# Kernel optimization log

Hardware: AMD Instinct MI355X
Metric: run time of the kernel (lower is better)

The kernel has to match this reference:

```python
import jax, jax.numpy as jnp
import numpy as np

B, IN_DIM, D, C = 16384, 1024, 256, 100


def setup_inputs() -> dict:
    key = jax.random.key(0)
    k1, k2, k3, k4 = jax.random.split(key, 4)
    x = jax.random.normal(k1, (B, IN_DIM), dtype=jnp.float32)
    W = jax.random.normal(k2, (IN_DIM, D), dtype=jnp.float32) * (1.0 / np.sqrt(IN_DIM))
    b = jax.random.normal(k3, (D,), dtype=jnp.float32) * 0.01
    P = jax.random.normal(k4, (C, D), dtype=jnp.float32)  # class prototypes [C, D]
    return {"x": x, "W": W, "b": b, "P": P}


def reference(x, W, b, P):
    # Encoder: Z = x @ W + b  -> [B, D]
    Z = x @ W + b
    d = Z.shape[-1]
    # MSE(r, p) = mean((r - p)^2) = (|r|^2 - 2 r.p + |p|^2) / D
    # Computed via expansion to avoid the [B, C, D] broadcast intermediate.
    sq = (
        jnp.sum(Z * Z, axis=-1, keepdims=True)      # [B, 1]
        - 2.0 * (Z @ P.T)                            # [B, C]
        + jnp.sum(P * P, axis=-1)[None, :]           # [1, C]
    )
    return -sq / d  # [B, C]
```

## Files before the change

### kernel.cpp

```cpp
#include <hip/hip_runtime.h>

#define BATCH 16384
#define KDIM  1024
#define DDIM  256
#define CNUM  100
#define CPAD  112
#define RSTR  72

typedef __bf16 bf16x8 __attribute__((ext_vector_type(8)));
typedef float  floatx4 __attribute__((ext_vector_type(4)));

static __device__ __forceinline__ unsigned short f2b(float f) {
    return __builtin_bit_cast(unsigned short, (__bf16)f);
}

__global__ __launch_bounds__(256) void prep(const float* __restrict__ W,
                                            const float* __restrict__ P,
                                            unsigned short* __restrict__ Wt2,
                                            unsigned short* __restrict__ Pbf,
                                            float* __restrict__ pnorm2) {
    __shared__ float T[32][33];
    const int bid = blockIdx.x;
    if (bid < 256) {
        const int k0 = (bid & 31) * 32;
        const int n0 = (bid >> 5) * 32;
        const int j  = threadIdx.x & 31;
        const int i0 = threadIdx.x >> 5;
#pragma unroll
        for (int l = 0; l < 4; ++l) {
            int i = i0 + l * 8;
            T[i][j] = W[(k0 + i) * DDIM + n0 + j];
        }
        __syncthreads();
        if (threadIdx.x < 128) {
            const int l  = threadIdx.x & 63;
            const int fn = threadIdx.x >> 6;
            const int lm = l & 15, lq = l >> 4;
            bf16x8 v;
#pragma unroll
            for (int jj = 0; jj < 8; ++jj)
                v[jj] = (__bf16)T[lq * 8 + jj][fn * 16 + lm];
            const int nblk = (n0 >> 4) + fn;
            const int kblk = k0 >> 5;
            *(bf16x8*)&Wt2[(nblk * 32 + kblk) * 512 + l * 8] = v;
        }
    } else {
        const int wave = threadIdx.x >> 6;
        const int lane = threadIdx.x & 63;
        const int c = (bid - 256) * 4 + wave;
        float s = 0.f;
#pragma unroll
        for (int jj = 0; jj < 4; ++jj) {
            int d = jj * 64 + lane;
            float v = (c < CNUM) ? P[c * DDIM + d] : 0.f;
            Pbf[c * DDIM + d] = f2b(v);
            s += v * v;
        }
#pragma unroll
        for (int m = 1; m < 64; m <<= 1) s += __shfl_xor(s, m, 64);
        if (lane == 0) pnorm2[c] = s;
    }
}

#define KSTEP(KK, CUR, NXT, P0, P1, P2, P3)                                    \
    {                                                                          \
        const unsigned short* As_c = U16 + (CUR) * 8192 + kh * 4096;           \
        const int kb_ = (KK) >> 5;                                             \
        if ((KK) + 64 < 512) {                                                 \
            _Pragma("unroll")                                                  \
            for (int kf = 0; kf < 2; ++kf) {                                   \
                _Pragma("unroll")                                              \
                for (int f = 0; f < 4; ++f)                                    \
                    b[NXT][kf * 4 + f] = *(const bf16x8*)(gB + f * 16384 +     \
                                                     (kb_ + 2 + kf) * 512);    \
            }                                                                  \
            bf16x8 ha;                                                         \
            ha[0] = (__bf16)P0[0]; ha[1] = (__bf16)P0[1];                      \
            ha[2] = (__bf16)P0[2]; ha[3] = (__bf16)P0[3];                      \
            ha[4] = (__bf16)P1[0]; ha[5] = (__bf16)P1[1];                      \
            ha[6] = (__bf16)P1[2]; ha[7] = (__bf16)P1[3];                      \
            *(bf16x8*)&U16[(NXT) * 8192 + ldsA] = ha;                          \
            bf16x8 hb;                                                         \
            hb[0] = (__bf16)P2[0]; hb[1] = (__bf16)P2[1];                      \
            hb[2] = (__bf16)P2[2]; hb[3] = (__bf16)P2[3];                      \
            hb[4] = (__bf16)P3[0]; hb[5] = (__bf16)P3[1];                      \
            hb[6] = (__bf16)P3[2]; hb[7] = (__bf16)P3[3];                      \
            *(bf16x8*)&U16[(NXT) * 8192 + 4096 + ldsA] = hb;                   \
            if ((KK) + 192 < 512) {                                            \
                P0 = *(const floatx4*)(gA + (KK) + 192);                       \
                P1 = *(const floatx4*)(gA + (KK) + 196);                       \
                P2 = *(const floatx4*)(gA + 512 + (KK) + 192);                 \
                P3 = *(const floatx4*)(gA + 512 + (KK) + 196);                 \
            }                                                                  \
        }                                                                      \
        _Pragma("unroll")                                                      \
        for (int kf = 0; kf < 2; ++kf) {                                       \
            const int sw = kf ? sw1 : sw0;                                     \
            bf16x8 a0 = *(const bf16x8*)&As_c[lm * 64 + sw];                   \
            bf16x8 a1 = *(const bf16x8*)&As_c[(16 + lm) * 64 + sw];            \
            bf16x8 a2 = *(const bf16x8*)&As_c[(32 + lm) * 64 + sw];            \
            bf16x8 a3 = *(const bf16x8*)&As_c[(48 + lm) * 64 + sw];            \
            _Pragma("unroll")                                                  \
            for (int f = 0; f < 4; ++f) {                                      \
                acc[0][f] = __builtin_amdgcn_mfma_f32_16x16x32_bf16(           \
                    a0, b[CUR][kf * 4 + f], acc[0][f], 0, 0, 0);               \
                acc[1][f] = __builtin_amdgcn_mfma_f32_16x16x32_bf16(           \
                    a1, b[CUR][kf * 4 + f], acc[1][f], 0, 0, 0);               \
                acc[2][f] = __builtin_amdgcn_mfma_f32_16x16x32_bf16(           \
                    a2, b[CUR][kf * 4 + f], acc[2][f], 0, 0, 0);               \
                acc[3][f] = __builtin_amdgcn_mfma_f32_16x16x32_bf16(           \
                    a3, b[CUR][kf * 4 + f], acc[3][f], 0, 0, 0);               \
            }                                                                  \
        }                                                                      \
        asm volatile("s_waitcnt lgkmcnt(0)\n\ts_barrier" ::: "memory");        \
    }

__global__ __launch_bounds__(512, 2) void fused_main(
    const float* __restrict__ x, const float* __restrict__ bias,
    const unsigned short* __restrict__ Wt2, const unsigned short* __restrict__ Pbf,
    const float* __restrict__ pnorm2, float* __restrict__ out)
{
    __shared__ __align__(16) float Ubuf[4 * 64 * RSTR];
    __shared__ float rn2[4][64];
    unsigned short* U16 = (unsigned short*)Ubuf;
    float* Rs = Ubuf;
    unsigned short* Zs = (unsigned short*)Ubuf;

    const int tid  = threadIdx.x;
    const int wave = tid >> 6;
    const int kh   = wave >> 2;
    const int wn   = wave & 3;
    const int lane = tid & 63;
    const int lm   = lane & 15;
    const int lq   = lane >> 4;
    const int r0   = blockIdx.x * 64;

    const int rowA = tid >> 3;
    const int kbA  = tid & 7;
    const float* gA = x + (size_t)(r0 + rowA) * KDIM + kbA * 8;
    const int ldsA = rowA * 64 + ((kbA ^ (rowA & 7)) * 8);

    const unsigned short* gB = Wt2 + wn * 65536 + kh * 8192 + lane * 8;

    const int sw0 = ((0 * 4 + lq) ^ (lm & 7)) * 8;
    const int sw1 = ((1 * 4 + lq) ^ (lm & 7)) * 8;

    floatx4 acc[4][4];
#pragma unroll
    for (int g = 0; g < 4; ++g)
#pragma unroll
        for (int f = 0; f < 4; ++f) { acc[g][f][0]=0.f; acc[g][f][1]=0.f; acc[g][f][2]=0.f; acc[g][f][3]=0.f; }

    bf16x8 b[2][8];

    {
        floatx4 q0 = *(const floatx4*)(gA);
        floatx4 q1 = *(const floatx4*)(gA + 4);
        floatx4 q2 = *(const floatx4*)(gA + 512);
        floatx4 q3 = *(const floatx4*)(gA + 516);
        bf16x8 ha;
        ha[0] = (__bf16)q0[0]; ha[1] = (__bf16)q0[1];
        ha[2] = (__bf16)q0[2]; ha[3] = (__bf16)q0[3];
        ha[4] = (__bf16)q1[0]; ha[5] = (__bf16)q1[1];
        ha[6] = (__bf16)q1[2]; ha[7] = (__bf16)q1[3];
        *(bf16x8*)&U16[ldsA] = ha;
        bf16x8 hb;
        hb[0] = (__bf16)q2[0]; hb[1] = (__bf16)q2[1];
        hb[2] = (__bf16)q2[2]; hb[3] = (__bf16)q2[3];
        hb[4] = (__bf16)q3[0]; hb[5] = (__bf16)q3[1];
        hb[6] = (__bf16)q3[2]; hb[7] = (__bf16)q3[3];
        *(bf16x8*)&U16[4096 + ldsA] = hb;
    }
#pragma unroll
    for (int kf = 0; kf < 2; ++kf)
#pragma unroll
        for (int f = 0; f < 4; ++f)
            b[0][kf * 4 + f] = *(const bf16x8*)(gB + f * 16384 + kf * 512);
    floatx4 pa0 = *(const floatx4*)(gA + 64);
    floatx4 pa1 = *(const floatx4*)(gA + 68);
    floatx4 pa2 = *(const floatx4*)(gA + 576);
    floatx4 pa3 = *(const floatx4*)(gA + 580);
    floatx4 pb0 = *(const floatx4*)(gA + 128);
    floatx4 pb1 = *(const floatx4*)(gA + 132);
    floatx4 pb2 = *(const floatx4*)(gA + 640);
    floatx4 pb3 = *(const floatx4*)(gA + 644);
    asm volatile("s_waitcnt lgkmcnt(0)\n\ts_barrier" ::: "memory");

    for (int kk0 = 0; kk0 < 512; kk0 += 128) {
        KSTEP(kk0,      0, 1, pa0, pa1, pa2, pa3)
        KSTEP(kk0 + 64, 1, 0, pb0, pb1, pb2, pb3)
    }

    if (kh == 1) {
#pragma unroll
        for (int g = 0; g < 4; ++g)
#pragma unroll
            for (int f = 0; f < 4; ++f)
                *(floatx4*)&Rs[(wn * 64 + f * 16 + lm) * RSTR + g * 16 + lq * 4] = acc[g][f];
    }
    __syncthreads();
    if (kh == 0) {
#pragma unroll
        for (int g = 0; g < 4; ++g)
#pragma unroll
            for (int f = 0; f < 4; ++f) {
                floatx4 p = *(const floatx4*)&Rs[(wn * 64 + f * 16 + lm) * RSTR + g * 16 + lq * 4];
#pragma unroll
                for (int r = 0; r < 4; ++r) acc[g][f][r] += p[r];
            }
#pragma unroll
        for (int f = 0; f < 4; ++f) {
            float bb = bias[wn * 64 + f * 16 + lm];
#pragma unroll
            for (int g = 0; g < 4; ++g)
#pragma unroll
                for (int r = 0; r < 4; ++r) acc[g][f][r] += bb;
        }
#pragma unroll
        for (int g = 0; g < 4; ++g) {
            float s0 = 0.f, s1 = 0.f, s2 = 0.f, s3 = 0.f;
#pragma unroll
            for (int f = 0; f < 4; ++f) {
                s0 += acc[g][f][0] * acc[g][f][0];
                s1 += acc[g][f][1] * acc[g][f][1];
                s2 += acc[g][f][2] * acc[g][f][2];
                s3 += acc[g][f][3] * acc[g][f][3];
            }
#pragma unroll
            for (int m = 1; m < 16; m <<= 1) {
                s0 += __shfl_xor(s0, m, 64);
                s1 += __shfl_xor(s1, m, 64);
                s2 += __shfl_xor(s2, m, 64);
                s3 += __shfl_xor(s3, m, 64);
            }
            if (lm == 0) {
                int rl = g * 16 + lq * 4;
                rn2[wn][rl + 0] = s0;
                rn2[wn][rl + 1] = s1;
                rn2[wn][rl + 2] = s2;
                rn2[wn][rl + 3] = s3;
            }
        }
    }
    __syncthreads();

    if (kh == 0) {
#pragma unroll
        for (int g = 0; g < 4; ++g)
#pragma unroll
            for (int f = 0; f < 4; ++f) {
                int col = wn * 64 + f * 16 + lm;
#pragma unroll
                for (int r = 0; r < 4; ++r)
                    Zs[(g * 16 + lq * 4 + r) * 264 + col] = f2b(acc[g][f][r]);
            }
    }
    __syncthreads();

    {
        const int ct = wave;
        if (ct < 7) {
            floatx4 acc2[4];
#pragma unroll
            for (int nf = 0; nf < 4; ++nf) { acc2[nf][0]=0.f; acc2[nf][1]=0.f; acc2[nf][2]=0.f; acc2[nf][3]=0.f; }
            const unsigned short* gP = Pbf + (ct * 16 + lm) * DDIM + lq * 8;
#pragma unroll
            for (int ks = 0; ks < 8; ++ks) {
                bf16x8 ap = *(const bf16x8*)(gP + ks * 32);
#pragma unroll
                for (int nf = 0; nf < 4; ++nf) {
                    bf16x8 bz = *(const bf16x8*)&Zs[(nf * 16 + lm) * 264 + ks * 32 + lq * 8];
                    acc2[nf] = __builtin_amdgcn_mfma_f32_16x16x32_bf16(ap, bz, acc2[nf], 0, 0, 0);
                }
            }
            int c0 = ct * 16 + lq * 4;
            if (c0 < CNUM) {
                floatx4 pn = *(const floatx4*)(pnorm2 + c0);
#pragma unroll
                for (int nf = 0; nf < 4; ++nf) {
                    int rl = nf * 16 + lm;
                    float rn = rn2[0][rl] + rn2[1][rl] + rn2[2][rl] + rn2[3][rl];
                    floatx4 o;
#pragma unroll
                    for (int r = 0; r < 4; ++r)
                        o[r] = (2.f * acc2[nf][r] - rn - pn[r]) * (1.f / 256.f);
                    *(floatx4*)&out[(r0 + rl) * CNUM + c0] = o;
                }
            }
        }
    }
}

extern "C" void kernel_launch(void* const* d_in, const int* in_sizes, int n_in,
                              void* d_out, int out_size, void* d_ws, size_t ws_size,
                              hipStream_t stream) {
    const float* x = (const float*)d_in[0];
    const float* W = (const float*)d_in[1];
    const float* b = (const float*)d_in[2];
    const float* P = (const float*)d_in[3];
    float* out = (float*)d_out;

    unsigned short* Wt2 = (unsigned short*)d_ws;
    unsigned short* Pbf = Wt2 + KDIM * DDIM;
    float* pn2 = (float*)(Pbf + CPAD * DDIM);

    prep<<<256 + CPAD / 4, 256, 0, stream>>>(W, P, Wt2, Pbf, pn2);
    fused_main<<<BATCH / 64, 512, 0, stream>>>(x, b, Wt2, Pbf, pn2, out);
}
```

Baseline: 112.1 us.

## Halve row tile to 32 rows per block and raise occupancy to four blocks

Each block now handles 32 batch rows instead of 64, which halves the accumulator registers, the A-tile LDS buffers and the staged x loads. The grid doubles and launch bounds ask for four blocks per CU to improve latency hiding. In exchange, each W fragment loaded from global memory now feeds half as many MFMAs, so W traffic per output row doubles and per-block fixed overheads (barriers, reductions, P loads) are spread over fewer rows.

Result: slower. 114.4 us (+2.1%).

```diff
diff --git a/kernel.cpp b/kernel.cpp
--- a/kernel.cpp
+++ b/kernel.cpp
@@ -5,7 +5,7 @@
 #define DDIM  256
 #define CNUM  100
 #define CPAD  112
-#define RSTR  72
+#define RSTR  36
 
 typedef __bf16 bf16x8 __attribute__((ext_vector_type(8)));
 typedef float  floatx4 __attribute__((ext_vector_type(4)));
@@ -62,9 +62,9 @@
     }
 }
 
-#define KSTEP(KK, CUR, NXT, P0, P1, P2, P3)                                    \
+#define KSTEP(KK, CUR, NXT, P0, P1)                                            \
     {                                                                          \
-        const unsigned short* As_c = U16 + (CUR) * 8192 + kh * 4096;           \
+        const unsigned short* As_c = U16 + (CUR) * 4096 + kh * 2048;           \
         const int kb_ = (KK) >> 5;                                             \
         if ((KK) + 64 < 512) {                                                 \
             _Pragma("unroll")                                                  \
@@ -79,18 +79,10 @@
             ha[2] = (__bf16)P0[2]; ha[3] = (__bf16)P0[3];                      \
             ha[4] = (__bf16)P1[0]; ha[5] = (__bf16)P1[1];                      \
             ha[6] = (__bf16)P1[2]; ha[7] = (__bf16)P1[3];                      \
-            *(bf16x8*)&U16[(NXT) * 8192 + ldsA] = ha;                          \
-            bf16x8 hb;                                                         \
-            hb[0] = (__bf16)P2[0]; hb[1] = (__bf16)P2[1];                      \
-            hb[2] = (__bf16)P2[2]; hb[3] = (__bf16)P2[3];                      \
-            hb[4] = (__bf16)P3[0]; hb[5] = (__bf16)P3[1];                      \
-            hb[6] = (__bf16)P3[2]; hb[7] = (__bf16)P3[3];                      \
-            *(bf16x8*)&U16[(NXT) * 8192 + 4096 + ldsA] = hb;                   \
+            *(bf16x8*)&U16[(NXT) * 4096 + thT * 2048 + ldsA] = ha;             \
             if ((KK) + 192 < 512) {                                            \
                 P0 = *(const floatx4*)(gA + (KK) + 192);                       \
                 P1 = *(const floatx4*)(gA + (KK) + 196);                       \
-                P2 = *(const floatx4*)(gA + 512 + (KK) + 192);                 \
-                P3 = *(const floatx4*)(gA + 512 + (KK) + 196);                 \
             }                                                                  \
         }                                                                      \
         _Pragma("unroll")                                                      \
@@ -98,30 +90,24 @@
             const int sw = kf ? sw1 : sw0;                                     \
             bf16x8 a0 = *(const bf16x8*)&As_c[lm * 64 + sw];                   \
             bf16x8 a1 = *(const bf16x8*)&As_c[(16 + lm) * 64 + sw];            \
-            bf16x8 a2 = *(const bf16x8*)&As_c[(32 + lm) * 64 + sw];            \
-            bf16x8 a3 = *(const bf16x8*)&As_c[(48 + lm) * 64 + sw];            \
             _Pragma("unroll")                                                  \
             for (int f = 0; f < 4; ++f) {                                      \
                 acc[0][f] = __builtin_amdgcn_mfma_f32_16x16x32_bf16(           \
                     a0, b[CUR][kf * 4 + f], acc[0][f], 0, 0, 0);               \
                 acc[1][f] = __builtin_amdgcn_mfma_f32_16x16x32_bf16(           \
                     a1, b[CUR][kf * 4 + f], acc[1][f], 0, 0, 0);               \
-                acc[2][f] = __builtin_amdgcn_mfma_f32_16x16x32_bf16(           \
-                    a2, b[CUR][kf * 4 + f], acc[2][f], 0, 0, 0);               \
-                acc[3][f] = __builtin_amdgcn_mfma_f32_16x16x32_bf16(           \
-                    a3, b[CUR][kf * 4 + f], acc[3][f], 0, 0, 0);               \
             }                                                                  \
         }                                                                      \
         asm volatile("s_waitcnt lgkmcnt(0)\n\ts_barrier" ::: "memory");        \
     }
 
-__global__ __launch_bounds__(512, 2) void fused_main(
+__global__ __launch_bounds__(512, 4) void fused_main(
     const float* __restrict__ x, const float* __restrict__ bias,
     const unsigned short* __restrict__ Wt2, const unsigned short* __restrict__ Pbf,
     const float* __restrict__ pnorm2, float* __restrict__ out)
 {
-    __shared__ __align__(16) float Ubuf[4 * 64 * RSTR];
-    __shared__ float rn2[4][64];
+    __shared__ __align__(16) float Ubuf[DDIM * RSTR];
+    __shared__ float rn2[4][32];
     unsigned short* U16 = (unsigned short*)Ubuf;
     float* Rs = Ubuf;
     unsigned short* Zs = (unsigned short*)Ubuf;
@@ -133,11 +119,12 @@
     const int lane = tid & 63;
     const int lm   = lane & 15;
     const int lq   = lane >> 4;
-    const int r0   = blockIdx.x * 64;
-
-    const int rowA = tid >> 3;
+    const int r0   = blockIdx.x * 32;
+
+    const int thT  = tid >> 8;
+    const int rowA = (tid & 255) >> 3;
     const int kbA  = tid & 7;
-    const float* gA = x + (size_t)(r0 + rowA) * KDIM + kbA * 8;
+    const float* gA = x + (size_t)(r0 + rowA) * KDIM + thT * 512 + kbA * 8;
     const int ldsA = rowA * 64 + ((kbA ^ (rowA & 7)) * 8);
 
     const unsigned short* gB = Wt2 + wn * 65536 + kh * 8192 + lane * 8;
@@ -145,9 +132,9 @@
     const int sw0 = ((0 * 4 + lq) ^ (lm & 7)) * 8;
     const int sw1 = ((1 * 4 + lq) ^ (lm & 7)) * 8;
 
-    floatx4 acc[4][4];
-#pragma unroll
-    for (int g = 0; g < 4; ++g)
+    floatx4 acc[2][4];
+#pragma unroll
+    for (int g = 0; g < 2; ++g)
 #pragma unroll
         for (int f = 0; f < 4; ++f) { acc[g][f][0]=0.f; acc[g][f][1]=0.f; acc[g][f][2]=0.f; acc[g][f][3]=0.f; }
 
@@ -156,20 +143,12 @@
     {
         floatx4 q0 = *(const floatx4*)(gA);
         floatx4 q1 = *(const floatx4*)(gA + 4);
-        floatx4 q2 = *(const floatx4*)(gA + 512);
-        floatx4 q3 = *(const floatx4*)(gA + 516);
         bf16x8 ha;
         ha[0] = (__bf16)q0[0]; ha[1] = (__bf16)q0[1];
         ha[2] = (__bf16)q0[2]; ha[3] = (__bf16)q0[3];
         ha[4] = (__bf16)q1[0]; ha[5] = (__bf16)q1[1];
         ha[6] = (__bf16)q1[2]; ha[7] = (__bf16)q1[3];
-        *(bf16x8*)&U16[ldsA] = ha;
-        bf16x8 hb;
-        hb[0] = (__bf16)q2[0]; hb[1] = (__bf16)q2[1];
-        hb[2] = (__bf16)q2[2]; hb[3] = (__bf16)q2[3];
-        hb[4] = (__bf16)q3[0]; hb[5] = (__bf16)q3[1];
-        hb[6] = (__bf16)q3[2]; hb[7] = (__bf16)q3[3];
-        *(bf16x8*)&U16[4096 + ldsA] = hb;
+        *(bf16x8*)&U16[thT * 2048 + ldsA] = ha;
     }
 #pragma unroll
     for (int kf = 0; kf < 2; ++kf)
@@ -178,22 +157,18 @@
             b[0][kf * 4 + f] = *(const bf16x8*)(gB + f * 16384 + kf * 512);
     floatx4 pa0 = *(const floatx4*)(gA + 64);
     floatx4 pa1 = *(const floatx4*)(gA + 68);
-    floatx4 pa2 = *(const floatx4*)(gA + 576);
-    floatx4 pa3 = *(const floatx4*)(gA + 580);
     floatx4 pb0 = *(const floatx4*)(gA + 128);
     floatx4 pb1 = *(const floatx4*)(gA + 132);
-    floatx4 pb2 = *(const floatx4*)(gA + 640);
-    floatx4 pb3 = *(const floatx4*)(gA + 644);
     asm volatile("s_waitcnt lgkmcnt(0)\n\ts_barrier" ::: "memory");
 
     for (int kk0 = 0; kk0 < 512; kk0 += 128) {
-        KSTEP(kk0,      0, 1, pa0, pa1, pa2, pa3)
-        KSTEP(kk0 + 64, 1, 0, pb0, pb1, pb2, pb3)
+        KSTEP(kk0,      0, 1, pa0, pa1)
+        KSTEP(kk0 + 64, 1, 0, pb0, pb1)
     }
 
     if (kh == 1) {
 #pragma unroll
-        for (int g = 0; g < 4; ++g)
+        for (int g = 0; g < 2; ++g)
 #pragma unroll
             for (int f = 0; f < 4; ++f)
                 *(floatx4*)&Rs[(wn * 64 + f * 16 + lm) * RSTR + g * 16 + lq * 4] = acc[g][f];
@@ -201,7 +176,7 @@
     __syncthreads();
     if (kh == 0) {
 #pragma unroll
-        for (int g = 0; g < 4; ++g)
+        for (int g = 0; g < 2; ++g)
 #pragma unroll
             for (int f = 0; f < 4; ++f) {
                 floatx4 p = *(const floatx4*)&Rs[(wn * 64 + f * 16 + lm) * RSTR + g * 16 + lq * 4];
@@ -212,12 +187,12 @@
         for (int f = 0; f < 4; ++f) {
             float bb = bias[wn * 64 + f * 16 + lm];
 #pragma unroll
-            for (int g = 0; g < 4; ++g)
+            for (int g = 0; g < 2; ++g)
 #pragma unroll
                 for (int r = 0; r < 4; ++r) acc[g][f][r] += bb;
         }
 #pragma unroll
-        for (int g = 0; g < 4; ++g) {
+        for (int g = 0; g < 2; ++g) {
             float s0 = 0.f, s1 = 0.f, s2 = 0.f, s3 = 0.f;
 #pragma unroll
             for (int f = 0; f < 4; ++f) {
@@ -246,7 +221,7 @@
 
     if (kh == 0) {
 #pragma unroll
-        for (int g = 0; g < 4; ++g)
+        for (int g = 0; g < 2; ++g)
 #pragma unroll
             for (int f = 0; f < 4; ++f) {
                 int col = wn * 64 + f * 16 + lm;
@@ -260,15 +235,15 @@
     {
         const int ct = wave;
         if (ct < 7) {
-            floatx4 acc2[4];
-#pragma unroll
-            for (int nf = 0; nf < 4; ++nf) { acc2[nf][0]=0.f; acc2[nf][1]=0.f; acc2[nf][2]=0.f; acc2[nf][3]=0.f; }
+            floatx4 acc2[2];
+#pragma unroll
+            for (int nf = 0; nf < 2; ++nf) { acc2[nf][0]=0.f; acc2[nf][1]=0.f; acc2[nf][2]=0.f; acc2[nf][3]=0.f; }
             const unsigned short* gP = Pbf + (ct * 16 + lm) * DDIM + lq * 8;
 #pragma unroll
             for (int ks = 0; ks < 8; ++ks) {
                 bf16x8 ap = *(const bf16x8*)(gP + ks * 32);
 #pragma unroll
-                for (int nf = 0; nf < 4; ++nf) {
+                for (int nf = 0; nf < 2; ++nf) {
                     bf16x8 bz = *(const bf16x8*)&Zs[(nf * 16 + lm) * 264 + ks * 32 + lq * 8];
                     acc2[nf] = __builtin_amdgcn_mfma_f32_16x16x32_bf16(ap, bz, acc2[nf], 0, 0, 0);
                 }
@@ -277,7 +252,7 @@
             if (c0 < CNUM) {
                 floatx4 pn = *(const floatx4*)(pnorm2 + c0);
 #pragma unroll
-                for (int nf = 0; nf < 4; ++nf) {
+                for (int nf = 0; nf < 2; ++nf) {
                     int rl = nf * 16 + lm;
                     float rn = rn2[0][rl] + rn2[1][rl] + rn2[2][rl] + rn2[3][rl];
                     floatx4 o;
@@ -305,5 +280,5 @@
     float* pn2 = (float*)(Pbf + CPAD * DDIM);
 
     prep<<<256 + CPAD / 4, 256, 0, stream>>>(W, P, Wt2, Pbf, pn2);
-    fused_main<<<BATCH / 64, 512, 0, stream>>>(x, b, Wt2, Pbf, pn2, out);
-}
+    fused_main<<<BATCH / 32, 512, 0, stream>>>(x, b, Wt2, Pbf, pn2, out);
+}
```

## Double block to 1024 threads, splitting the D dimension across eight waves

Applied to the files above, without the earlier changes.

Grows each workgroup from 8 to 16 waves. Each wave now owns 32 output columns instead of 64, while the two K-halves are kept. The x tile load is split between the two thread halves, per-wave register accumulators and B fragments are halved, and the row-norm partials now cover 8 column groups. This aims to raise latency hiding and occupancy per CU, at the cost of more barrier participants and less B reuse per wave.

Result: no change. 112.1 us (+0.1%).

```diff
diff --git a/kernel.cpp b/kernel.cpp
--- a/kernel.cpp
+++ b/kernel.cpp
@@ -5,7 +5,7 @@
 #define DDIM  256
 #define CNUM  100
 #define CPAD  112
-#define RSTR  72
+#define RSTR  68
 
 typedef __bf16 bf16x8 __attribute__((ext_vector_type(8)));
 typedef float  floatx4 __attribute__((ext_vector_type(4)));
@@ -62,7 +62,7 @@
     }
 }
 
-#define KSTEP(KK, CUR, NXT, P0, P1, P2, P3)                                    \
+#define KSTEP(KK, CUR, NXT, P0, P1)                                            \
     {                                                                          \
         const unsigned short* As_c = U16 + (CUR) * 8192 + kh * 4096;           \
         const int kb_ = (KK) >> 5;                                             \
@@ -70,8 +70,8 @@
             _Pragma("unroll")                                                  \
             for (int kf = 0; kf < 2; ++kf) {                                   \
                 _Pragma("unroll")                                              \
-                for (int f = 0; f < 4; ++f)                                    \
-                    b[NXT][kf * 4 + f] = *(const bf16x8*)(gB + f * 16384 +     \
+                for (int f = 0; f < 2; ++f)                                    \
+                    b[NXT][kf * 2 + f] = *(const bf16x8*)(gB + f * 16384 +     \
                                                      (kb_ + 2 + kf) * 512);    \
             }                                                                  \
             bf16x8 ha;                                                         \
@@ -80,17 +80,9 @@
             ha[4] = (__bf16)P1[0]; ha[5] = (__bf16)P1[1];                      \
             ha[6] = (__bf16)P1[2]; ha[7] = (__bf16)P1[3];                      \
             *(bf16x8*)&U16[(NXT) * 8192 + ldsA] = ha;                          \
-            bf16x8 hb;                                                         \
-            hb[0] = (__bf16)P2[0]; hb[1] = (__bf16)P2[1];                      \
-            hb[2] = (__bf16)P2[2]; hb[3] = (__bf16)P2[3];                      \
-            hb[4] = (__bf16)P3[0]; hb[5] = (__bf16)P3[1];                      \
-            hb[6] = (__bf16)P3[2]; hb[7] = (__bf16)P3[3];                      \
-            *(bf16x8*)&U16[(NXT) * 8192 + 4096 + ldsA] = hb;                   \
             if ((KK) + 192 < 512) {                                            \
                 P0 = *(const floatx4*)(gA + (KK) + 192);                       \
                 P1 = *(const floatx4*)(gA + (KK) + 196);                       \
-                P2 = *(const floatx4*)(gA + 512 + (KK) + 192);                 \
-                P3 = *(const floatx4*)(gA + 512 + (KK) + 196);                 \
             }                                                                  \
         }                                                                      \
         _Pragma("unroll")                                                      \
@@ -101,116 +93,105 @@
             bf16x8 a2 = *(const bf16x8*)&As_c[(32 + lm) * 64 + sw];            \
             bf16x8 a3 = *(const bf16x8*)&As_c[(48 + lm) * 64 + sw];            \
             _Pragma("unroll")                                                  \
-            for (int f = 0; f < 4; ++f) {                                      \
+            for (int f = 0; f < 2; ++f) {                                      \
                 acc[0][f] = __builtin_amdgcn_mfma_f32_16x16x32_bf16(           \
-                    a0, b[CUR][kf * 4 + f], acc[0][f], 0, 0, 0);               \
+                    a0, b[CUR][kf * 2 + f], acc[0][f], 0, 0, 0);               \
                 acc[1][f] = __builtin_amdgcn_mfma_f32_16x16x32_bf16(           \
-                    a1, b[CUR][kf * 4 + f], acc[1][f], 0, 0, 0);               \
+                    a1, b[CUR][kf * 2 + f], acc[1][f], 0, 0, 0);               \
                 acc[2][f] = __builtin_amdgcn_mfma_f32_16x16x32_bf16(           \
-                    a2, b[CUR][kf * 4 + f], acc[2][f], 0, 0, 0);               \
+                    a2, b[CUR][kf * 2 + f], acc[2][f], 0, 0, 0);               \
                 acc[3][f] = __builtin_amdgcn_mfma_f32_16x16x32_bf16(           \
-                    a3, b[CUR][kf * 4 + f], acc[3][f], 0, 0, 0);               \
+                    a3, b[CUR][kf * 2 + f], acc[3][f], 0, 0, 0);               \
             }                                                                  \
         }                                                                      \
         asm volatile("s_waitcnt lgkmcnt(0)\n\ts_barrier" ::: "memory");        \
     }
 
-__global__ __launch_bounds__(512, 2) void fused_main(
+__global__ __launch_bounds__(1024, 4) void fused_main(
     const float* __restrict__ x, const float* __restrict__ bias,
     const unsigned short* __restrict__ Wt2, const unsigned short* __restrict__ Pbf,
     const float* __restrict__ pnorm2, float* __restrict__ out)
 {
-    __shared__ __align__(16) float Ubuf[4 * 64 * RSTR];
-    __shared__ float rn2[4][64];
+    __shared__ __align__(16) float Ubuf[DDIM * RSTR];
+    __shared__ float rn2[8][64];
     unsigned short* U16 = (unsigned short*)Ubuf;
     float* Rs = Ubuf;
     unsigned short* Zs = (unsigned short*)Ubuf;
 
     const int tid  = threadIdx.x;
     const int wave = tid >> 6;
-    const int kh   = wave >> 2;
-    const int wn   = wave & 3;
+    const int kh   = wave >> 3;
+    const int wn   = wave & 7;
     const int lane = tid & 63;
     const int lm   = lane & 15;
     const int lq   = lane >> 4;
     const int r0   = blockIdx.x * 64;
 
-    const int rowA = tid >> 3;
+    const int half = tid >> 9;
+    const int rowA = (tid >> 3) & 63;
     const int kbA  = tid & 7;
-    const float* gA = x + (size_t)(r0 + rowA) * KDIM + kbA * 8;
-    const int ldsA = rowA * 64 + ((kbA ^ (rowA & 7)) * 8);
-
-    const unsigned short* gB = Wt2 + wn * 65536 + kh * 8192 + lane * 8;
+    const float* gA = x + (size_t)(r0 + rowA) * KDIM + half * 512 + kbA * 8;
+    const int ldsA = half * 4096 + rowA * 64 + ((kbA ^ (rowA & 7)) * 8);
+
+    const unsigned short* gB = Wt2 + wn * 32768 + kh * 8192 + lane * 8;
 
     const int sw0 = ((0 * 4 + lq) ^ (lm & 7)) * 8;
     const int sw1 = ((1 * 4 + lq) ^ (lm & 7)) * 8;
 
-    floatx4 acc[4][4];
+    floatx4 acc[4][2];
 #pragma unroll
     for (int g = 0; g < 4; ++g)
 #pragma unroll
-        for (int f = 0; f < 4; ++f) { acc[g][f][0]=0.f; acc[g][f][1]=0.f; acc[g][f][2]=0.f; acc[g][f][3]=0.f; }
-
-    bf16x8 b[2][8];
+        for (int f = 0; f < 2; ++f) { acc[g][f][0]=0.f; acc[g][f][1]=0.f; acc[g][f][2]=0.f; acc[g][f][3]=0.f; }
+
+    bf16x8 b[2][4];
 
     {
         floatx4 q0 = *(const floatx4*)(gA);
         floatx4 q1 = *(const floatx4*)(gA + 4);
-        floatx4 q2 = *(const floatx4*)(gA + 512);
-        floatx4 q3 = *(const floatx4*)(gA + 516);
         bf16x8 ha;
         ha[0] = (__bf16)q0[0]; ha[1] = (__bf16)q0[1];
         ha[2] = (__bf16)q0[2]; ha[3] = (__bf16)q0[3];
         ha[4] = (__bf16)q1[0]; ha[5] = (__bf16)q1[1];
         ha[6] = (__bf16)q1[2]; ha[7] = (__bf16)q1[3];
         *(bf16x8*)&U16[ldsA] = ha;
-        bf16x8 hb;
-        hb[0] = (__bf16)q2[0]; hb[1] = (__bf16)q2[1];
-        hb[2] = (__bf16)q2[2]; hb[3] = (__bf16)q2[3];
-        hb[4] = (__bf16)q3[0]; hb[5] = (__bf16)q3[1];
-        hb[6] = (__bf16)q3[2]; hb[7] = (__bf16)q3[3];
-        *(bf16x8*)&U16[4096 + ldsA] = hb;
     }
 #pragma unroll
     for (int kf = 0; kf < 2; ++kf)
 #pragma unroll
-        for (int f = 0; f < 4; ++f)
-            b[0][kf * 4 + f] = *(const bf16x8*)(gB + f * 16384 + kf * 512);
+        for (int f = 0; f < 2; ++f)
+            b[0][kf * 2 + f] = *(const bf16x8*)(gB + f * 16384 + kf * 512);
     floatx4 pa0 = *(const floatx4*)(gA + 64);
     floatx4 pa1 = *(const floatx4*)(gA + 68);
-    floatx4 pa2 = *(const floatx4*)(gA + 576);
-    floatx4 pa3 = *(const floatx4*)(gA + 580);
     floatx4 pb0 = *(const floatx4*)(gA + 128);
     floatx4 pb1 = *(const floatx4*)(gA + 132);
-    floatx4 pb2 = *(const floatx4*)(gA + 640);
-    floatx4 pb3 = *(const floatx4*)(gA + 644);
     asm volatile("s_waitcnt lgkmcnt(0)\n\ts_barrier" ::: "memory");
 
     for (int kk0 = 0; kk0 < 512; kk0 += 128) {
-        KSTEP(kk0,      0, 1, pa0, pa1, pa2, pa3)
-        KSTEP(kk0 + 64, 1, 0, pb0, pb1, pb2, pb3)
+        KSTEP(kk0,      0, 1, pa0, pa1)
+        KSTEP(kk0 + 64, 1, 0, pb0, pb1)
     }
 
     if (kh == 1) {
 #pragma unroll
         for (int g = 0; g < 4; ++g)
 #pragma unroll
-            for (int f = 0; f < 4; ++f)
-                *(floatx4*)&Rs[(wn * 64 + f * 16 + lm) * RSTR + g * 16 + lq * 4] = acc[g][f];
+            for (int f = 0; f < 2; ++f)
+                *(floatx4*)&Rs[(wn * 32 + f * 16 + lm) * RSTR + g * 16 + lq * 4] = acc[g][f];
     }
     __syncthreads();
     if (kh == 0) {
 #pragma unroll
         for (int g = 0; g < 4; ++g)
 #pragma unroll
-            for (int f = 0; f < 4; ++f) {
-                floatx4 p = *(const floatx4*)&Rs[(wn * 64 + f * 16 + lm) * RSTR + g * 16 + lq * 4];
+            for (int f = 0; f < 2; ++f) {
+                floatx4 p = *(const floatx4*)&Rs[(wn * 32 + f * 16 + lm) * RSTR + g * 16 + lq * 4];
 #pragma unroll
                 for (int r = 0; r < 4; ++r) acc[g][f][r] += p[r];
             }
 #pragma unroll
-        for (int f = 0; f < 4; ++f) {
-            float bb = bias[wn * 64 + f * 16 + lm];
+        for (int f = 0; f < 2; ++f) {
+            float bb = bias[wn * 32 + f * 16 + lm];
 #pragma unroll
             for (int g = 0; g < 4; ++g)
 #pragma unroll
@@ -220,7 +201,7 @@
         for (int g = 0; g < 4; ++g) {
             float s0 = 0.f, s1 = 0.f, s2 = 0.f, s3 = 0.f;
 #pragma unroll
-            for (int f = 0; f < 4; ++f) {
+            for (int f = 0; f < 2; ++f) {
                 s0 += acc[g][f][0] * acc[g][f][0];
                 s1 += acc[g][f][1] * acc[g][f][1];
                 s2 += acc[g][f][2] * acc[g][f][2];
@@ -248,8 +229,8 @@
 #pragma unroll
         for (int g = 0; g < 4; ++g)
 #pragma unroll
-            for (int f = 0; f < 4; ++f) {
-                int col = wn * 64 + f * 16 + lm;
+            for (int f = 0; f < 2; ++f) {
+                int col = wn * 32 + f * 16 + lm;
 #pragma unroll
                 for (int r = 0; r < 4; ++r)
                     Zs[(g * 16 + lq * 4 + r) * 264 + col] = f2b(acc[g][f][r]);
@@ -279,7 +260,8 @@
 #pragma unroll
                 for (int nf = 0; nf < 4; ++nf) {
                     int rl = nf * 16 + lm;
-                    float rn = rn2[0][rl] + rn2[1][rl] + rn2[2][rl] + rn2[3][rl];
+                    float rn = rn2[0][rl] + rn2[1][rl] + rn2[2][rl] + rn2[3][rl]
+                             + rn2[4][rl] + rn2[5][rl] + rn2[6][rl] + rn2[7][rl];
                     floatx4 o;
 #pragma unroll
                     for (int r = 0; r < 4; ++r)
@@ -305,5 +287,5 @@
     float* pn2 = (float*)(Pbf + CPAD * DDIM);
 
     prep<<<256 + CPAD / 4, 256, 0, stream>>>(W, P, Wt2, Pbf, pn2);
-    fused_main<<<BATCH / 64, 512, 0, stream>>>(x, b, Wt2, Pbf, pn2, out);
-}
+    fused_main<<<BATCH / 64, 1024, 0, stream>>>(x, b, Wt2, Pbf, pn2, out);
+}
```

## Double the LDS K-tile per barrier and decouple W register prefetch granularity

Applied to the files above, without the earlier changes.

Restructures the main GEMM loop so each LDS stage holds 128 K-columns of x instead of 64. This halves the number of workgroup barriers to four, with each stage computed as two register-granule steps. W fragments are now prefetched two granules ahead, with the load issued right after the granule's MFMAs, and the swizzle is widened to 16 chunks per row. The cost is a larger LDS footprint (enlarged to the residual buffer size) and more live prefetch registers, which may pressure occupancy at 2 waves/SIMD.

Result: no change. 110.9 us (-1.0%).

```diff
diff --git a/kernel.cpp b/kernel.cpp
--- a/kernel.cpp
+++ b/kernel.cpp
@@ -62,56 +62,65 @@
     }
 }
 
-#define KSTEP(KK, CUR, NXT, P0, P1, P2, P3)                                    \
+#define CVT8(H, A_, B_)                                                        \
+    H[0] = (__bf16)A_[0]; H[1] = (__bf16)A_[1];                                \
+    H[2] = (__bf16)A_[2]; H[3] = (__bf16)A_[3];                                \
+    H[4] = (__bf16)B_[0]; H[5] = (__bf16)B_[1];                                \
+    H[6] = (__bf16)B_[2]; H[7] = (__bf16)B_[3];
+
+#define MFMA_(A_, B_, C_) __builtin_amdgcn_mfma_f32_16x16x32_bf16(A_, B_, C_, 0, 0, 0)
+
+#define GRAN(G, CUR)                                                           \
     {                                                                          \
-        const unsigned short* As_c = U16 + (CUR) * 8192 + kh * 4096;           \
-        const int kb_ = (KK) >> 5;                                             \
-        if ((KK) + 64 < 512) {                                                 \
+        const unsigned short* As_c = U16 + (CUR) * 16384 + kh * 8192;          \
+        _Pragma("unroll")                                                      \
+        for (int kf = 0; kf < 2; ++kf) {                                       \
+            const int sw = ((((G) & 1) * 8 + kf * 4 + lq) ^ lm) * 8;           \
+            bf16x8 a0 = *(const bf16x8*)&As_c[lm * 128 + sw];                  \
+            bf16x8 a1 = *(const bf16x8*)&As_c[(16 + lm) * 128 + sw];           \
+            bf16x8 a2 = *(const bf16x8*)&As_c[(32 + lm) * 128 + sw];           \
+            bf16x8 a3 = *(const bf16x8*)&As_c[(48 + lm) * 128 + sw];           \
             _Pragma("unroll")                                                  \
-            for (int kf = 0; kf < 2; ++kf) {                                   \
+            for (int f = 0; f < 4; ++f) {                                      \
+                acc[0][f] = MFMA_(a0, b[(G) & 1][kf * 4 + f], acc[0][f]);      \
+                acc[1][f] = MFMA_(a1, b[(G) & 1][kf * 4 + f], acc[1][f]);      \
+                acc[2][f] = MFMA_(a2, b[(G) & 1][kf * 4 + f], acc[2][f]);      \
+                acc[3][f] = MFMA_(a3, b[(G) & 1][kf * 4 + f], acc[3][f]);      \
+            }                                                                  \
+        }                                                                      \
+        if ((G) + 2 < 8) {                                                     \
+            _Pragma("unroll")                                                  \
+            for (int kf = 0; kf < 2; ++kf)                                     \
                 _Pragma("unroll")                                              \
                 for (int f = 0; f < 4; ++f)                                    \
-                    b[NXT][kf * 4 + f] = *(const bf16x8*)(gB + f * 16384 +     \
-                                                     (kb_ + 2 + kf) * 512);    \
-            }                                                                  \
-            bf16x8 ha;                                                         \
-            ha[0] = (__bf16)P0[0]; ha[1] = (__bf16)P0[1];                      \
-            ha[2] = (__bf16)P0[2]; ha[3] = (__bf16)P0[3];                      \
-            ha[4] = (__bf16)P1[0]; ha[5] = (__bf16)P1[1];                      \
-            ha[6] = (__bf16)P1[2]; ha[7] = (__bf16)P1[3];                      \
-            *(bf16x8*)&U16[(NXT) * 8192 + ldsA] = ha;                          \
-            bf16x8 hb;                                                         \
-            hb[0] = (__bf16)P2[0]; hb[1] = (__bf16)P2[1];                      \
-            hb[2] = (__bf16)P2[2]; hb[3] = (__bf16)P2[3];                      \
-            hb[4] = (__bf16)P3[0]; hb[5] = (__bf16)P3[1];                      \
-            hb[6] = (__bf16)P3[2]; hb[7] = (__bf16)P3[3];                      \
-            *(bf16x8*)&U16[(NXT) * 8192 + 4096 + ldsA] = hb;                   \
-            if ((KK) + 192 < 512) {                                            \
-                P0 = *(const floatx4*)(gA + (KK) + 192);                       \
-                P1 = *(const floatx4*)(gA + (KK) + 196);                       \
-                P2 = *(const floatx4*)(gA + 512 + (KK) + 192);                 \
-                P3 = *(const floatx4*)(gA + 512 + (KK) + 196);                 \
+                    b[(G) & 1][kf * 4 + f] = *(const bf16x8*)(gB +             \
+                        f * 16384 + (((G) + 2) * 2 + kf) * 512);               \
+        }                                                                      \
+    }
+
+#define PAIRSTEP(T, CUR, NXT)                                                  \
+    {                                                                          \
+        if ((T) < 3) {                                                         \
+            bf16x8 h0, h1, h2, h3;                                             \
+            CVT8(h0, p[0], p[1]) CVT8(h1, p[2], p[3])                          \
+            CVT8(h2, p[4], p[5]) CVT8(h3, p[6], p[7])                          \
+            *(bf16x8*)&U16[(NXT) * 16384 + ldsW0] = h0;                        \
+            *(bf16x8*)&U16[(NXT) * 16384 + ldsW1] = h1;                        \
+            *(bf16x8*)&U16[(NXT) * 16384 + 8192 + ldsW0] = h2;                 \
+            *(bf16x8*)&U16[(NXT) * 16384 + 8192 + ldsW1] = h3;                 \
+            if ((T) < 2) {                                                     \
+                p[0] = *(const floatx4*)(gA + ((T) + 2) * 128);                \
+                p[1] = *(const floatx4*)(gA + ((T) + 2) * 128 + 4);            \
+                p[2] = *(const floatx4*)(gA + ((T) + 2) * 128 + 64);           \
+                p[3] = *(const floatx4*)(gA + ((T) + 2) * 128 + 68);           \
+                p[4] = *(const floatx4*)(gA + 512 + ((T) + 2) * 128);          \
+                p[5] = *(const floatx4*)(gA + 512 + ((T) + 2) * 128 + 4);      \
+                p[6] = *(const floatx4*)(gA + 512 + ((T) + 2) * 128 + 64);     \
+                p[7] = *(const floatx4*)(gA + 512 + ((T) + 2) * 128 + 68);     \
             }                                                                  \
         }                                                                      \
-        _Pragma("unroll")                                                      \
-        for (int kf = 0; kf < 2; ++kf) {                                       \
-            const int sw = kf ? sw1 : sw0;                                     \
-            bf16x8 a0 = *(const bf16x8*)&As_c[lm * 64 + sw];                   \
-            bf16x8 a1 = *(const bf16x8*)&As_c[(16 + lm) * 64 + sw];            \
-            bf16x8 a2 = *(const bf16x8*)&As_c[(32 + lm) * 64 + sw];            \
-            bf16x8 a3 = *(const bf16x8*)&As_c[(48 + lm) * 64 + sw];            \
-            _Pragma("unroll")                                                  \
-            for (int f = 0; f < 4; ++f) {                                      \
-                acc[0][f] = __builtin_amdgcn_mfma_f32_16x16x32_bf16(           \
-                    a0, b[CUR][kf * 4 + f], acc[0][f], 0, 0, 0);               \
-                acc[1][f] = __builtin_amdgcn_mfma_f32_16x16x32_bf16(           \
-                    a1, b[CUR][kf * 4 + f], acc[1][f], 0, 0, 0);               \
-                acc[2][f] = __builtin_amdgcn_mfma_f32_16x16x32_bf16(           \
-                    a2, b[CUR][kf * 4 + f], acc[2][f], 0, 0, 0);               \
-                acc[3][f] = __builtin_amdgcn_mfma_f32_16x16x32_bf16(           \
-                    a3, b[CUR][kf * 4 + f], acc[3][f], 0, 0, 0);               \
-            }                                                                  \
-        }                                                                      \
+        GRAN(2 * (T), CUR)                                                     \
+        GRAN(2 * (T) + 1, CUR)                                                 \
         asm volatile("s_waitcnt lgkmcnt(0)\n\ts_barrier" ::: "memory");        \
     }
 
@@ -120,7 +129,7 @@
     const unsigned short* __restrict__ Wt2, const unsigned short* __restrict__ Pbf,
     const float* __restrict__ pnorm2, float* __restrict__ out)
 {
-    __shared__ __align__(16) float Ubuf[4 * 64 * RSTR];
+    __shared__ __align__(16) float Ubuf[DDIM * RSTR];
     __shared__ float rn2[4][64];
     unsigned short* U16 = (unsigned short*)Ubuf;
     float* Rs = Ubuf;
@@ -138,58 +147,57 @@
     const int rowA = tid >> 3;
     const int kbA  = tid & 7;
     const float* gA = x + (size_t)(r0 + rowA) * KDIM + kbA * 8;
-    const int ldsA = rowA * 64 + ((kbA ^ (rowA & 7)) * 8);
+    const int ldsW0 = rowA * 128 + ((kbA ^ (rowA & 15)) * 8);
+    const int ldsW1 = rowA * 128 + (((kbA + 8) ^ (rowA & 15)) * 8);
 
     const unsigned short* gB = Wt2 + wn * 65536 + kh * 8192 + lane * 8;
 
-    const int sw0 = ((0 * 4 + lq) ^ (lm & 7)) * 8;
-    const int sw1 = ((1 * 4 + lq) ^ (lm & 7)) * 8;
-
     floatx4 acc[4][4];
 #pragma unroll
     for (int g = 0; g < 4; ++g)
 #pragma unroll
         for (int f = 0; f < 4; ++f) { acc[g][f][0]=0.f; acc[g][f][1]=0.f; acc[g][f][2]=0.f; acc[g][f][3]=0.f; }
 
-    bf16x8 b[2][8];
+    bf16x8  b[2][8];
+    floatx4 p[8];
 
     {
         floatx4 q0 = *(const floatx4*)(gA);
         floatx4 q1 = *(const floatx4*)(gA + 4);
-        floatx4 q2 = *(const floatx4*)(gA + 512);
-        floatx4 q3 = *(const floatx4*)(gA + 516);
-        bf16x8 ha;
-        ha[0] = (__bf16)q0[0]; ha[1] = (__bf16)q0[1];
-        ha[2] = (__bf16)q0[2]; ha[3] = (__bf16)q0[3];
-        ha[4] = (__bf16)q1[0]; ha[5] = (__bf16)q1[1];
-        ha[6] = (__bf16)q1[2]; ha[7] = (__bf16)q1[3];
-        *(bf16x8*)&U16[ldsA] = ha;
-        bf16x8 hb;
-        hb[0] = (__bf16)q2[0]; hb[1] = (__bf16)q2[1];
-        hb[2] = (__bf16)q2[2]; hb[3] = (__bf16)q2[3];
-        hb[4] = (__bf16)q3[0]; hb[5] = (__bf16)q3[1];
-        hb[6] = (__bf16)q3[2]; hb[7] = (__bf16)q3[3];
-        *(bf16x8*)&U16[4096 + ldsA] = hb;
+        floatx4 q2 = *(const floatx4*)(gA + 64);
+        floatx4 q3 = *(const floatx4*)(gA + 68);
+        floatx4 q4 = *(const floatx4*)(gA + 512);
+        floatx4 q5 = *(const floatx4*)(gA + 516);
+        floatx4 q6 = *(const floatx4*)(gA + 576);
+        floatx4 q7 = *(const floatx4*)(gA + 580);
+        bf16x8 h0, h1, h2, h3;
+        CVT8(h0, q0, q1) CVT8(h1, q2, q3) CVT8(h2, q4, q5) CVT8(h3, q6, q7)
+        *(bf16x8*)&U16[ldsW0] = h0;
+        *(bf16x8*)&U16[ldsW1] = h1;
+        *(bf16x8*)&U16[8192 + ldsW0] = h2;
+        *(bf16x8*)&U16[8192 + ldsW1] = h3;
     }
 #pragma unroll
     for (int kf = 0; kf < 2; ++kf)
 #pragma unroll
-        for (int f = 0; f < 4; ++f)
+        for (int f = 0; f < 4; ++f) {
             b[0][kf * 4 + f] = *(const bf16x8*)(gB + f * 16384 + kf * 512);
-    floatx4 pa0 = *(const floatx4*)(gA + 64);
-    floatx4 pa1 = *(const floatx4*)(gA + 68);
-    floatx4 pa2 = *(const floatx4*)(gA + 576);
-    floatx4 pa3 = *(const floatx4*)(gA + 580);
-    floatx4 pb0 = *(const floatx4*)(gA + 128);
-    floatx4 pb1 = *(const floatx4*)(gA + 132);
-    floatx4 pb2 = *(const floatx4*)(gA + 640);
-    floatx4 pb3 = *(const floatx4*)(gA + 644);
+            b[1][kf * 4 + f] = *(const bf16x8*)(gB + f * 16384 + (2 + kf) * 512);
+        }
+    p[0] = *(const floatx4*)(gA + 128);
+    p[1] = *(const floatx4*)(gA + 132);
+    p[2] = *(const floatx4*)(gA + 192);
+    p[3] = *(const floatx4*)(gA + 196);
+    p[4] = *(const floatx4*)(gA + 640);
+    p[5] = *(const floatx4*)(gA + 644);
+    p[6] = *(const floatx4*)(gA + 704);
+    p[7] = *(const floatx4*)(gA + 708);
     asm volatile("s_waitcnt lgkmcnt(0)\n\ts_barrier" ::: "memory");
 
-    for (int kk0 = 0; kk0 < 512; kk0 += 128) {
-        KSTEP(kk0,      0, 1, pa0, pa1, pa2, pa3)
-        KSTEP(kk0 + 64, 1, 0, pb0, pb1, pb2, pb3)
-    }
+    PAIRSTEP(0, 0, 1)
+    PAIRSTEP(1, 1, 0)
+    PAIRSTEP(2, 0, 1)
+    PAIRSTEP(3, 1, 0)
 
     if (kh == 1) {
 #pragma unroll
@@ -204,9 +212,9 @@
         for (int g = 0; g < 4; ++g)
 #pragma unroll
             for (int f = 0; f < 4; ++f) {
-                floatx4 p = *(const floatx4*)&Rs[(wn * 64 + f * 16 + lm) * RSTR + g * 16 + lq * 4];
-#pragma unroll
-                for (int r = 0; r < 4; ++r) acc[g][f][r] += p[r];
+                floatx4 pp = *(const floatx4*)&Rs[(wn * 64 + f * 16 + lm) * RSTR + g * 16 + lq * 4];
+#pragma unroll
+                for (int r = 0; r < 4; ++r) acc[g][f][r] += pp[r];
             }
 #pragma unroll
         for (int f = 0; f < 4; ++f) {
```
